# Kernel optimization log

Hardware: AMD Instinct MI355X
Metric: run time of the kernel (lower is better)

Reference implementation:

```python
import jax, jax.numpy as jnp
import numpy as np

# Scalar quantization params (QLinear __init__ args)
FEATURE_BITWIDTH = 8
WEIGHT_BITWIDTH = 8
INPUT_ZERO_POINT = -3
OUTPUT_ZERO_POINT = -5
INPUT_SCALE = 0.05
OUTPUT_SCALE = 0.1
QMIN = -(1 << (FEATURE_BITWIDTH - 1))   # -128
QMAX = (1 << (FEATURE_BITWIDTH - 1)) - 1  # 127

M, K, N = 8192, 4096, 4096


def float_to_fixed_point(x, bitwidth):
    """Represent x (0 < x < 1) as int_scale * 2^-frac_bits with int_scale
    in [2^(bitwidth-2), 2^(bitwidth-1)) (mantissa fits in signed `bitwidth` bits)."""
    frac_bits = (bitwidth - 1 - jnp.ceil(jnp.log2(x))).astype(jnp.int32)
    int_scale = jnp.round(x * jnp.exp2(frac_bits.astype(jnp.float32))).astype(jnp.int32)
    return int_scale, frac_bits


def setup_inputs() -> dict:
    key = jax.random.key(0)
    k1, k2, k3, k4 = jax.random.split(key, 4)
    qinput = jax.random.randint(k1, (M, K), -128, 128, dtype=jnp.int8)
    qweight = jax.random.randint(k2, (N, K), -128, 128, dtype=jnp.int8)
    qbias = jax.random.randint(k3, (N,), -(1 << 16), 1 << 16, dtype=jnp.int32)
    # per-output-channel weight scale; keeps folded scale in (0, 1)
    weight_scale = jax.random.uniform(k4, (N,), jnp.float32, 0.002, 0.02)
    return {"qinput": qinput, "qweight": qweight, "qbias": qbias,
            "weight_scale": weight_scale}


def reference(qinput, qweight, qbias, weight_scale):
    w32 = qweight.astype(jnp.int32)                      # [N, K]
    # Qbias' = qbias - sum_k(qweight) * Zin  (bias shift folding input zero point)
    shifted_qbias = qbias - w32.sum(axis=1) * INPUT_ZERO_POINT  # [N]
    # int32 GEMM: [M, K] @ [K, N] + bias
    acc = qinput.astype(jnp.int32) @ w32.T + shifted_qbias[None, :]  # [M, N]
    # fixed-point requantization: (acc * int_scale) >> frac_bits + Zout
    folded_scale = INPUT_SCALE * weight_scale / OUTPUT_SCALE         # [N], in (0,1)
    int_scale, frac_bits = float_to_fixed_point(folded_scale, FEATURE_BITWIDTH)
    # widen to int64 for the multiply so the (acc * int_scale) product cannot wrap
    prod = acc.astype(jnp.int64) * int_scale.astype(jnp.int64)[None, :]
    scaled = jnp.right_shift(prod, frac_bits.astype(jnp.int64)[None, :])  # arithmetic >>
    out = scaled + OUTPUT_ZERO_POINT
    return jnp.clip(out, QMIN, QMAX).astype(jnp.int8)
```

## Files before the change

### kernel.cpp

```cpp
#include <hip/hip_runtime.h>
#include <cstdint>
#include <cstddef>

#define M_DIM 8192
#define N_DIM 4096
#define K_DIM 4096

#define BM 128
#define BN 128
#define BK 128

#define BM2 256
#define BN2 256
#define BK2 128
#define NKT (K_DIM / BK2)

typedef int int32x4  __attribute__((ext_vector_type(4)));
typedef int int32x16 __attribute__((ext_vector_type(16)));


typedef __attribute__((address_space(1))) const void* gas_cptr;
typedef __attribute__((address_space(3))) void* las_ptr;

__device__ __forceinline__ void async_copy16(const void* g, void* l) {
    __builtin_amdgcn_global_load_lds((gas_cptr)g, (las_ptr)l, 16, 0, 0);
}

__device__ __forceinline__ int32x4 pack16(const int* p) {
    const int32x4* v = (const int32x4*)p;
    int32x4 w0 = v[0], w1 = v[1], w2 = v[2], w3 = v[3];
    int32x4 r;
    r.x = (w0.x & 0xFF) | ((w0.y & 0xFF) << 8) | ((w0.z & 0xFF) << 16) | (w0.w << 24);
    r.y = (w1.x & 0xFF) | ((w1.y & 0xFF) << 8) | ((w1.z & 0xFF) << 16) | (w1.w << 24);
    r.z = (w2.x & 0xFF) | ((w2.y & 0xFF) << 8) | ((w2.z & 0xFF) << 16) | (w2.w << 24);
    r.w = (w3.x & 0xFF) | ((w3.y & 0xFF) << 8) | ((w3.z & 0xFF) << 16) | (w3.w << 24);
    return r;
}

__global__ void ql_detect_kernel(const int* a, const int* b, int* ws) {
    int t = threadIdx.x;
    int fa = 0, fb = 0;
    for (int i = t; i < 4096; i += 64) {
        int va = a[i]; if (va > 127 || va < -128) fa = 1;
        int vb = b[i]; if (vb > 127 || vb < -128) fb = 1;
    }
    unsigned long long ba = __ballot(fa);
    unsigned long long bb = __ballot(fb);
    if (t == 0) { ws[0] = ba ? 1 : 0; ws[1] = bb ? 1 : 0; }
}

#define PACK_WBLOCKS 4096
__global__ __launch_bounds__(256)
void ql_pack2_kernel(const void* wsrc, int* wdst, const void* asrc, int* adst,
                     const int* ws) {
    const int fA = __builtin_amdgcn_readfirstlane(ws[0]);
    const int fW = __builtin_amdgcn_readfirstlane(ws[1]);
    const int bid = blockIdx.x;
    const int32x4* src;
    int32x4* dst;
    long base;
    if (bid < PACK_WBLOCKS) {
        if (fW) return;
        src = (const int32x4*)wsrc; dst = (int32x4*)wdst;
        base = (long)bid * 1024;
    } else {
        if (fA) return;
        src = (const int32x4*)asrc; dst = (int32x4*)adst;
        base = (long)(bid - PACK_WBLOCKS) * 1024;
    }
    const long d0 = base + (long)threadIdx.x * 4;
    int32x4 o;
#pragma unroll
    for (int k = 0; k < 4; ++k) {
        int32x4 v = src[d0 + k];
        ((int*)&o)[k] = (v.x & 0xFF) | ((v.y & 0xFF) << 8)
                      | ((v.z & 0xFF) << 16) | (v.w << 24);
    }
    dst[d0 >> 2] = o;
}

__global__ void ql_prep8_kernel(const void* worig, const int8_t* w8p, const int* qbias,
                                const float* wscale, int* ws) {
    const int fb = __builtin_amdgcn_readfirstlane(ws[1]);
    const int8_t* w8 = fb ? (const int8_t*)worig : w8p;

    const int lane = threadIdx.x & 63;
    const int wid  = threadIdx.x >> 6;
    const int n = blockIdx.x * 4 + wid;

    const int32x4* row = (const int32x4*)(w8 + (size_t)n * K_DIM);
    int s = 0;
    for (int c = lane; c < K_DIM / 16; c += 64) {
        int32x4 v = row[c];
#pragma unroll
        for (int j = 0; j < 4; ++j) {
            int w = (j == 0) ? v.x : (j == 1) ? v.y : (j == 2) ? v.z : v.w;
            s += (int)(int8_t)(w) + (int)(int8_t)(w >> 8)
               + (int)(int8_t)(w >> 16) + (w >> 24);
        }
    }
#pragma unroll
    for (int off = 32; off > 0; off >>= 1) s += __shfl_down(s, off, 64);

    if (lane == 0) {
        ws[16 + n] = qbias[n] + 3 * s;
        float folded = (0.05f * wscale[n]) / 0.1f;
        int fbits = (int)(7.0f - ceilf(log2f(folded)));
        int isc = (int)rintf(folded * exp2f((float)fbits));
        ws[16 + N_DIM + n] = isc;
        ws[16 + 2 * N_DIM + n] = fbits;
    }
}

__global__ void ql_prep_kernel(const void* wptr, const int* qbias,
                               const float* wscale, int* ws) {
    const int lane = threadIdx.x & 63;
    const int wid  = threadIdx.x >> 6;
    const int n = blockIdx.x * 4 + wid;
    const int b8 = __builtin_amdgcn_readfirstlane(ws[1]);

    int s = 0;
    if (b8) {
        const int32x4* row = (const int32x4*)((const int8_t*)wptr + (size_t)n * K_DIM);
        for (int c = lane; c < K_DIM / 16; c += 64) {
            int32x4 v = row[c];
#pragma unroll
            for (int j = 0; j < 4; ++j) {
                int w = (j == 0) ? v.x : (j == 1) ? v.y : (j == 2) ? v.z : v.w;
                s += (int)(int8_t)(w) + (int)(int8_t)(w >> 8)
                   + (int)(int8_t)(w >> 16) + (w >> 24);
            }
        }
    } else {
        const int32x4* row = (const int32x4*)((const int*)wptr + (size_t)n * K_DIM);
        for (int c = lane; c < K_DIM / 4; c += 64) {
            int32x4 v = row[c];
            s += v.x + v.y + v.z + v.w;
        }
    }
#pragma unroll
    for (int off = 32; off > 0; off >>= 1) s += __shfl_down(s, off, 64);

    if (lane == 0) {
        ws[16 + n] = qbias[n] + 3 * s;
        float folded = (0.05f * wscale[n]) / 0.1f;
        int fbits = (int)(7.0f - ceilf(log2f(folded)));
        int isc = (int)rintf(folded * exp2f((float)fbits));
        ws[16 + N_DIM + n] = isc;
        ws[16 + 2 * N_DIM + n] = fbits;
    }
}

__device__ __forceinline__ void ql_epilogue(int32x4 acc[4][4], const int* ws,
                                            int* out, int bm, int bn,
                                            int wm, int wn, int qm, int qh) {
    const int* qb  = ws + 16;
    const int* isc = ws + 16 + N_DIM;
    const int* fbt = ws + 16 + 2 * N_DIM;
#pragma unroll
    for (int j = 0; j < 4; ++j) {
        const int n_g = bn * BN + wn + j * 16 + qm;
        const int b0 = qb[n_g];
        const int s0 = isc[n_g];
        const int f0 = fbt[n_g];
#pragma unroll
        for (int i = 0; i < 4; ++i) {
            const int m_base = bm * BM + wm + i * 16 + qh * 4;
#pragma unroll
            for (int r = 0; r < 4; ++r) {
                int v = ((r == 0) ? acc[i][j].x : (r == 1) ? acc[i][j].y
                        : (r == 2) ? acc[i][j].z : acc[i][j].w) + b0;
                long long p = (long long)v * (long long)s0;
                int o = (int)(p >> f0) - 5;
                o = o < -128 ? -128 : (o > 127 ? 127 : o);
                out[(size_t)(m_base + r) * N_DIM + n_g] = o;
            }
        }
    }
}


#define TILE2(BUF, TT) do { \
    _Pragma("unroll") for (int ml = 0; ml < 2; ++ml) \
    _Pragma("unroll") for (int kc = 0; kc < 4; ++kc) \
        afL[ml][kc] = LA[BUF][baseAe[kc] + ml * 256]; \
    _Pragma("unroll") for (int kc = 0; kc < 4; ++kc) \
        bf0[kc] = LB[BUF][baseBe[kc]]; \
    _Pragma("unroll") for (int kc = 0; kc < 4; ++kc) \
        bf1[kc] = LB[BUF][baseBe[kc] + 256]; \
    _Pragma("unroll") for (int ml = 0; ml < 2; ++ml) \
    _Pragma("unroll") for (int kc = 0; kc < 4; ++kc) \
        afH[ml][kc] = LA[BUF][baseAe[kc] + 512 + ml * 256]; \
    if ((TT) + 1 < NKT) { \
        _Pragma("unroll") for (int h2 = 0; h2 < 4; ++h2) { \
            async_copy16(gA + (size_t)((TT) + 1) * 128 + (size_t)h2 * 262144, \
                         &LA[(BUF) ^ 1][h2 * 512 + t]); \
            async_copy16(gB + (size_t)((TT) + 1) * 128 + (size_t)h2 * 262144, \
                         &LB[(BUF) ^ 1][h2 * 512 + t]); \
        } \
    } \
    __builtin_amdgcn_s_setprio(1); \
    _Pragma("unroll") for (int kc = 0; kc < 4; ++kc) \
    _Pragma("unroll") for (int ml = 0; ml < 2; ++ml) \
        acc[ml][0] = __builtin_amdgcn_mfma_i32_32x32x32_i8(afL[ml][kc], bf0[kc], acc[ml][0], 0, 0, 0); \
    _Pragma("unroll") for (int kc = 0; kc < 4; ++kc) \
    _Pragma("unroll") for (int ml = 0; ml < 2; ++ml) \
        acc[ml][1] = __builtin_amdgcn_mfma_i32_32x32x32_i8(afL[ml][kc], bf1[kc], acc[ml][1], 0, 0, 0); \
    _Pragma("unroll") for (int kc = 0; kc < 4; ++kc) \
    _Pragma("unroll") for (int ml = 0; ml < 2; ++ml) \
        acc[2 + ml][0] = __builtin_amdgcn_mfma_i32_32x32x32_i8(afH[ml][kc], bf0[kc], acc[2 + ml][0], 0, 0, 0); \
    _Pragma("unroll") for (int kc = 0; kc < 4; ++kc) \
    _Pragma("unroll") for (int ml = 0; ml < 2; ++ml) \
        acc[2 + ml][1] = __builtin_amdgcn_mfma_i32_32x32x32_i8(afH[ml][kc], bf1[kc], acc[2 + ml][1], 0, 0, 0); \
    __builtin_amdgcn_s_setprio(0); \
    __syncthreads(); \
} while (0)

__global__ __launch_bounds__(512, 2)
void ql_gemm8_kernel(const void* a0, const int8_t* a8,
                     const void* b0, const int8_t* w8,
                     const int* ws, int* out) {
    __shared__ int32x4 LA[2][2048];
    __shared__ int32x4 LB[2][2048];

    const int fa = __builtin_amdgcn_readfirstlane(ws[0]);
    const int fb = __builtin_amdgcn_readfirstlane(ws[1]);
    const int8_t* aptr = fa ? (const int8_t*)a0 : a8;
    const int8_t* bptr = fb ? (const int8_t*)b0 : w8;

    const int t    = threadIdx.x;
    const int lane = t & 63;
    const int wid  = t >> 6;
    const int wr   = wid >> 2;
    const int wc   = wid & 3;
    const int l31  = lane & 31;
    const int hi   = lane >> 5;

    const int flat = blockIdx.y * gridDim.x + blockIdx.x;
    const int xcd  = flat & 7;
    const int lid  = flat >> 3;
    const int g    = lid >> 5;
    const int r    = lid & 31;
    const int bm   = xcd * 4 + g * 2 + (r & 1);
    const int bn   = r >> 1;

    const int arow0 = bm * BM2;
    const int brow0 = bn * BN2;

    const int fr = (lane & 7) ^ ((l31 >> 3) & 3);
    int baseAe[4], baseBe[4];
#pragma unroll
    for (int kc = 0; kc < 4; ++kc) {
        const int phys = (kc * 2 + hi) ^ fr;
        baseAe[kc] = (wr * 128 + l31) * 8 + phys;
        baseBe[kc] = (wc * 64  + l31) * 8 + phys;
    }

    const int colg = (t & 7) ^ ((t >> 3) & 7) ^ ((t >> 6) & 3);
    const int8_t* gA = aptr + (size_t)(arow0 + (t >> 3)) * K_DIM + colg * 16;
    const int8_t* gB = bptr + (size_t)(brow0 + (t >> 3)) * K_DIM + colg * 16;

    int32x16 acc[4][2] = {};
    int32x4 afL[2][4], afH[2][4], bf0[4], bf1[4];

#pragma unroll
    for (int h2 = 0; h2 < 4; ++h2) {
        async_copy16(gA + (size_t)h2 * 262144, &LA[0][h2 * 512 + t]);
        async_copy16(gB + (size_t)h2 * 262144, &LB[0][h2 * 512 + t]);
    }
    __syncthreads();

#pragma unroll 1
    for (int T = 0; T < NKT; T += 2) {
        TILE2(0, T);
        TILE2(1, T + 1);
    }

    const int* qb  = ws + 16;
    const int* isc = ws + 16 + N_DIM;
    const int* fbt = ws + 16 + 2 * N_DIM;
#pragma unroll
    for (int j = 0; j < 2; ++j) {
        const int n_g = bn * BN2 + wc * 64 + j * 32 + l31;
        const int b0r = qb[n_g];
        const int s0r = isc[n_g];
        const int f0r = fbt[n_g];
#pragma unroll
        for (int i = 0; i < 4; ++i) {
            const int m0 = bm * BM2 + wr * 128 + i * 32 + hi * 4;
#pragma unroll
            for (int reg = 0; reg < 16; ++reg) {
                const int row = (reg & 3) + 8 * (reg >> 2);
                int v = acc[i][j][reg] + b0r;
                long long p = (long long)v * (long long)s0r;
                int o = (int)(p >> f0r) - 5;
                o = o < -128 ? -128 : (o > 127 ? 127 : o);
                out[(size_t)(m0 + row) * N_DIM + n_g] = o;
            }
        }
    }
}

__global__ __launch_bounds__(256)
void ql_gemm_fb_kernel(const void* aptr, const void* bptr, const int* ws, int* out) {
    __shared__ int32x4 Als[BM * BK / 16];
    __shared__ int32x4 Bls[BN * BK / 16];

    const int a8 = __builtin_amdgcn_readfirstlane(ws[0]);
    const int b8 = __builtin_amdgcn_readfirstlane(ws[1]);

    const int t    = threadIdx.x;
    const int lane = t & 63;
    const int wid  = t >> 6;
    const int bn = blockIdx.x;
    const int bm = blockIdx.y;

    const int wm = (wid >> 1) * 64;
    const int wn = (wid & 1) * 64;
    const int qm = lane & 15;
    const int qh = lane >> 4;

    int32x4 acc[4][4] = {};

    for (int kt = 0; kt < K_DIM / BK; ++kt) {
        __syncthreads();
        const int k0 = kt * BK;
#pragma unroll
        for (int r = 0; r < 4; ++r) {
            const int c    = r * 256 + t;
            const int row  = c >> 3;
            const int colg = (c & 7) ^ (row & 7);
            const size_t offA = (size_t)(bm * BM + row) * K_DIM + k0 + colg * 16;
            const size_t offB = (size_t)(bn * BN + row) * K_DIM + k0 + colg * 16;
            if (a8) async_copy16((const int8_t*)aptr + offA, &Als[c]);
            else    Als[c] = pack16((const int*)aptr + offA);
            if (b8) async_copy16((const int8_t*)bptr + offB, &Bls[c]);
            else    Bls[c] = pack16((const int*)bptr + offB);
        }
        __syncthreads();

#pragma unroll
        for (int s = 0; s < 2; ++s) {
            const int colk = s * 4 + qh;
            int32x4 af[4], bf[4];
#pragma unroll
            for (int i = 0; i < 4; ++i) {
                const int ra = wm + i * 16 + qm;
                const int rb = wn + i * 16 + qm;
                af[i] = Als[ra * 8 + (colk ^ (ra & 7))];
                bf[i] = Bls[rb * 8 + (colk ^ (rb & 7))];
            }
#pragma unroll
            for (int i = 0; i < 4; ++i)
#pragma unroll
                for (int j = 0; j < 4; ++j)
                    acc[i][j] = __builtin_amdgcn_mfma_i32_16x16x64_i8(
                        af[i], bf[j], acc[i][j], 0, 0, 0);
        }
    }
    ql_epilogue(acc, ws, out, bm, bn, wm, wn, qm, qh);
}

extern "C" void kernel_launch(void* const* d_in, const int* in_sizes, int n_in,
                              void* d_out, int out_size, void* d_ws, size_t ws_size,
                              hipStream_t stream) {
    const void* qin    = d_in[0];
    const void* qwt    = d_in[1];
    const int* qbias   = (const int*)d_in[2];
    const float* wscal = (const float*)d_in[3];
    int* ws  = (int*)d_ws;
    int* out = (int*)d_out;

    hipLaunchKernelGGL(ql_detect_kernel, dim3(1), dim3(64), 0, stream,
                       (const int*)qin, (const int*)qwt, ws);

    const size_t need = 65536 + (size_t)M_DIM * K_DIM + (size_t)N_DIM * K_DIM;
    if (ws_size >= need) {
        int8_t* a8 = (int8_t*)d_ws + 65536;
        int8_t* w8 = a8 + (size_t)M_DIM * K_DIM;
        const unsigned packBlocks = PACK_WBLOCKS + (unsigned)((long)M_DIM * K_DIM / 4 / 1024);
        hipLaunchKernelGGL(ql_pack2_kernel, dim3(packBlocks), dim3(256),
                           0, stream, qwt, (int*)w8, qin, (int*)a8, ws);
        hipLaunchKernelGGL(ql_prep8_kernel, dim3(N_DIM / 4), dim3(256), 0, stream,
                           qwt, w8, qbias, wscal, ws);
        hipLaunchKernelGGL(ql_gemm8_kernel, dim3(N_DIM / BN2, M_DIM / BM2), dim3(512),
                           0, stream, qin, a8, qwt, w8, ws, out);
    } else {
        hipLaunchKernelGGL(ql_prep_kernel, dim3(N_DIM / 4), dim3(256), 0, stream,
                           qwt, qbias, wscal, ws);
        hipLaunchKernelGGL(ql_gemm_fb_kernel, dim3(N_DIM / BN, M_DIM / BM), dim3(256), 0, stream,
                           qin, qwt, ws, out);
    }
}
```

Baseline: 409.5 us.

## Fuse weight row-sum into pack kernel, deepen GEMM prefetch, nontemporal output stores

The weight-pack kernel now computes each row's sum and the requant parameters during packing, so the separate prep kernel exits early and does not re-read the packed weights. The GEMM main loop switches from one-stage-ahead double buffering with __syncthreads to two tiles in flight. It waits on vmcnt plus raw barriers and issues the next copy into the just-consumed buffer after the MFMAs. Output stores become nontemporal to avoid polluting cache. The risk is correctness of the manual vmcnt counts, since an async copy issues 8 per tile.

```diff
diff --git a/kernel.cpp b/kernel.cpp
--- a/kernel.cpp
+++ b/kernel.cpp
@@ -49,46 +49,66 @@
     if (t == 0) { ws[0] = ba ? 1 : 0; ws[1] = bb ? 1 : 0; }
 }
 
-#define PACK_WBLOCKS 4096
+#define PACK_WBLK 4096
+#define PACK_ABLK 8192
 __global__ __launch_bounds__(256)
 void ql_pack2_kernel(const void* wsrc, int* wdst, const void* asrc, int* adst,
-                     const int* ws) {
+                     const int* qbias, const float* wscale, int* ws) {
+    __shared__ int red[4];
     const int fA = __builtin_amdgcn_readfirstlane(ws[0]);
     const int fW = __builtin_amdgcn_readfirstlane(ws[1]);
     const int bid = blockIdx.x;
-    const int32x4* src;
-    int32x4* dst;
-    long base;
-    if (bid < PACK_WBLOCKS) {
+    const int tid = threadIdx.x;
+    if (bid < PACK_WBLK) {
         if (fW) return;
-        src = (const int32x4*)wsrc; dst = (int32x4*)wdst;
-        base = (long)bid * 1024;
+        const int n = bid;
+        const int32x4* src = (const int32x4*)wsrc + (size_t)n * 1024;
+        int* dst = wdst + (size_t)n * 1024;
+        int s = 0;
+#pragma unroll
+        for (int k = 0; k < 4; ++k) {
+            const int i = k * 256 + tid;
+            int32x4 v = src[i];
+            s += v.x + v.y + v.z + v.w;
+            dst[i] = (v.x & 0xFF) | ((v.y & 0xFF) << 8) | ((v.z & 0xFF) << 16) | (v.w << 24);
+        }
+#pragma unroll
+        for (int off = 32; off > 0; off >>= 1) s += __shfl_down(s, off, 64);
+        if ((tid & 63) == 0) red[tid >> 6] = s;
+        __syncthreads();
+        if (tid == 0) {
+            const int st = red[0] + red[1] + red[2] + red[3];
+            ws[16 + n] = qbias[n] + 3 * st;
+            float folded = (0.05f * wscale[n]) / 0.1f;
+            int fbits = (int)(7.0f - ceilf(log2f(folded)));
+            int isc = (int)rintf(folded * exp2f((float)fbits));
+            ws[16 + N_DIM + n] = isc;
+            ws[16 + 2 * N_DIM + n] = fbits;
+        }
     } else {
         if (fA) return;
-        src = (const int32x4*)asrc; dst = (int32x4*)adst;
-        base = (long)(bid - PACK_WBLOCKS) * 1024;
-    }
-    const long d0 = base + (long)threadIdx.x * 4;
-    int32x4 o;
-#pragma unroll
-    for (int k = 0; k < 4; ++k) {
-        int32x4 v = src[d0 + k];
-        ((int*)&o)[k] = (v.x & 0xFF) | ((v.y & 0xFF) << 8)
-                      | ((v.z & 0xFF) << 16) | (v.w << 24);
-    }
-    dst[d0 >> 2] = o;
-}
-
-__global__ void ql_prep8_kernel(const void* worig, const int8_t* w8p, const int* qbias,
+        const long base = (long)(bid - PACK_WBLK) * 1024;
+        const int32x4* src = (const int32x4*)asrc + base;
+        int* dst = adst + base;
+#pragma unroll
+        for (int k = 0; k < 4; ++k) {
+            const int i = k * 256 + tid;
+            int32x4 v = src[i];
+            dst[i] = (v.x & 0xFF) | ((v.y & 0xFF) << 8) | ((v.z & 0xFF) << 16) | (v.w << 24);
+        }
+    }
+}
+
+__global__ void ql_prep8_kernel(const void* worig, const int* qbias,
                                 const float* wscale, int* ws) {
     const int fb = __builtin_amdgcn_readfirstlane(ws[1]);
-    const int8_t* w8 = fb ? (const int8_t*)worig : w8p;
+    if (!fb) return;
 
     const int lane = threadIdx.x & 63;
     const int wid  = threadIdx.x >> 6;
     const int n = blockIdx.x * 4 + wid;
 
-    const int32x4* row = (const int32x4*)(w8 + (size_t)n * K_DIM);
+    const int32x4* row = (const int32x4*)((const int8_t*)worig + (size_t)n * K_DIM);
     int s = 0;
     for (int c = lane; c < K_DIM / 16; c += 64) {
         int32x4 v = row[c];
@@ -180,7 +200,9 @@
 }
 
 
-#define TILE2(BUF, TT) do { \
+#define TILE2(BUF, TT, VMC, DOST) do { \
+    asm volatile("s_waitcnt vmcnt(" #VMC ")" ::: "memory"); \
+    __builtin_amdgcn_s_barrier(); \
     _Pragma("unroll") for (int ml = 0; ml < 2; ++ml) \
     _Pragma("unroll") for (int kc = 0; kc < 4; ++kc) \
         afL[ml][kc] = LA[BUF][baseAe[kc] + ml * 256]; \
@@ -191,29 +213,29 @@
     _Pragma("unroll") for (int ml = 0; ml < 2; ++ml) \
     _Pragma("unroll") for (int kc = 0; kc < 4; ++kc) \
         afH[ml][kc] = LA[BUF][baseAe[kc] + 512 + ml * 256]; \
-    if ((TT) + 1 < NKT) { \
+    __builtin_amdgcn_s_setprio(1); \
+    _Pragma("unroll") for (int kc = 0; kc < 4; ++kc) \
+    _Pragma("unroll") for (int ml = 0; ml < 2; ++ml) \
+        acc[ml][0] = __builtin_amdgcn_mfma_i32_32x32x32_i8(afL[ml][kc], bf0[kc], acc[ml][0], 0, 0, 0); \
+    _Pragma("unroll") for (int kc = 0; kc < 4; ++kc) \
+    _Pragma("unroll") for (int ml = 0; ml < 2; ++ml) \
+        acc[ml][1] = __builtin_amdgcn_mfma_i32_32x32x32_i8(afL[ml][kc], bf1[kc], acc[ml][1], 0, 0, 0); \
+    _Pragma("unroll") for (int kc = 0; kc < 4; ++kc) \
+    _Pragma("unroll") for (int ml = 0; ml < 2; ++ml) \
+        acc[2 + ml][0] = __builtin_amdgcn_mfma_i32_32x32x32_i8(afH[ml][kc], bf0[kc], acc[2 + ml][0], 0, 0, 0); \
+    _Pragma("unroll") for (int kc = 0; kc < 4; ++kc) \
+    _Pragma("unroll") for (int ml = 0; ml < 2; ++ml) \
+        acc[2 + ml][1] = __builtin_amdgcn_mfma_i32_32x32x32_i8(afH[ml][kc], bf1[kc], acc[2 + ml][1], 0, 0, 0); \
+    __builtin_amdgcn_s_setprio(0); \
+    __builtin_amdgcn_s_barrier(); \
+    if (DOST) { \
         _Pragma("unroll") for (int h2 = 0; h2 < 4; ++h2) { \
-            async_copy16(gA + (size_t)((TT) + 1) * 128 + (size_t)h2 * 262144, \
-                         &LA[(BUF) ^ 1][h2 * 512 + t]); \
-            async_copy16(gB + (size_t)((TT) + 1) * 128 + (size_t)h2 * 262144, \
-                         &LB[(BUF) ^ 1][h2 * 512 + t]); \
+            async_copy16(gA + (size_t)((TT) + 2) * 128 + (size_t)h2 * 262144, \
+                         &LA[BUF][h2 * 512 + t]); \
+            async_copy16(gB + (size_t)((TT) + 2) * 128 + (size_t)h2 * 262144, \
+                         &LB[BUF][h2 * 512 + t]); \
         } \
     } \
-    __builtin_amdgcn_s_setprio(1); \
-    _Pragma("unroll") for (int kc = 0; kc < 4; ++kc) \
-    _Pragma("unroll") for (int ml = 0; ml < 2; ++ml) \
-        acc[ml][0] = __builtin_amdgcn_mfma_i32_32x32x32_i8(afL[ml][kc], bf0[kc], acc[ml][0], 0, 0, 0); \
-    _Pragma("unroll") for (int kc = 0; kc < 4; ++kc) \
-    _Pragma("unroll") for (int ml = 0; ml < 2; ++ml) \
-        acc[ml][1] = __builtin_amdgcn_mfma_i32_32x32x32_i8(afL[ml][kc], bf1[kc], acc[ml][1], 0, 0, 0); \
-    _Pragma("unroll") for (int kc = 0; kc < 4; ++kc) \
-    _Pragma("unroll") for (int ml = 0; ml < 2; ++ml) \
-        acc[2 + ml][0] = __builtin_amdgcn_mfma_i32_32x32x32_i8(afH[ml][kc], bf0[kc], acc[2 + ml][0], 0, 0, 0); \
-    _Pragma("unroll") for (int kc = 0; kc < 4; ++kc) \
-    _Pragma("unroll") for (int ml = 0; ml < 2; ++ml) \
-        acc[2 + ml][1] = __builtin_amdgcn_mfma_i32_32x32x32_i8(afH[ml][kc], bf1[kc], acc[2 + ml][1], 0, 0, 0); \
-    __builtin_amdgcn_s_setprio(0); \
-    __syncthreads(); \
 } while (0)
 
 __global__ __launch_bounds__(512, 2)
@@ -268,13 +290,19 @@
         async_copy16(gA + (size_t)h2 * 262144, &LA[0][h2 * 512 + t]);
         async_copy16(gB + (size_t)h2 * 262144, &LB[0][h2 * 512 + t]);
     }
-    __syncthreads();
+#pragma unroll
+    for (int h2 = 0; h2 < 4; ++h2) {
+        async_copy16(gA + 128 + (size_t)h2 * 262144, &LA[1][h2 * 512 + t]);
+        async_copy16(gB + 128 + (size_t)h2 * 262144, &LB[1][h2 * 512 + t]);
+    }
 
 #pragma unroll 1
-    for (int T = 0; T < NKT; T += 2) {
-        TILE2(0, T);
-        TILE2(1, T + 1);
-    }
+    for (int T = 0; T < NKT - 2; T += 2) {
+        TILE2(0, T, 8, true);
+        TILE2(1, T + 1, 8, true);
+    }
+    TILE2(0, NKT - 2, 8, false);
+    TILE2(1, NKT - 1, 0, false);
 
     const int* qb  = ws + 16;
     const int* isc = ws + 16 + N_DIM;
@@ -295,7 +323,7 @@
                 long long p = (long long)v * (long long)s0r;
                 int o = (int)(p >> f0r) - 5;
                 o = o < -128 ? -128 : (o > 127 ? 127 : o);
-                out[(size_t)(m0 + row) * N_DIM + n_g] = o;
+                __builtin_nontemporal_store(o, &out[(size_t)(m0 + row) * N_DIM + n_g]);
             }
         }
     }
@@ -378,11 +406,10 @@
     if (ws_size >= need) {
         int8_t* a8 = (int8_t*)d_ws + 65536;
         int8_t* w8 = a8 + (size_t)M_DIM * K_DIM;
-        const unsigned packBlocks = PACK_WBLOCKS + (unsigned)((long)M_DIM * K_DIM / 4 / 1024);
-        hipLaunchKernelGGL(ql_pack2_kernel, dim3(packBlocks), dim3(256),
-                           0, stream, qwt, (int*)w8, qin, (int*)a8, ws);
+        hipLaunchKernelGGL(ql_pack2_kernel, dim3(PACK_WBLK + PACK_ABLK), dim3(256),
+                           0, stream, qwt, (int*)w8, qin, (int*)a8, qbias, wscal, ws);
         hipLaunchKernelGGL(ql_prep8_kernel, dim3(N_DIM / 4), dim3(256), 0, stream,
-                           qwt, w8, qbias, wscal, ws);
+                           qwt, qbias, wscal, ws);
         hipLaunchKernelGGL(ql_gemm8_kernel, dim3(N_DIM / BN2, M_DIM / BM2), dim3(512),
                            0, stream, qin, a8, qwt, w8, ws, out);
     } else {
```

Measured after the change: 412.9 us. Within noise of the previous version (+0.8%).
